# Kernel optimization log

Hardware: AMD Instinct MI355X
Metric: run time of the kernel (lower is better)

The kernel has to match this reference:

```python
import jax, jax.numpy as jnp
import numpy as np
from jax import lax

B, L, E, P, K, KS, H, T = 64, 512, 256, 64, 512, 3, 512, 53
V, MAXL = 50000, 512


def _span_idx(k):
    ks, kl = jax.random.split(k)
    starts = jax.random.randint(ks, (B,), 1, L - 9)
    spans = jax.random.randint(kl, (B,), 0, 8)
    return jnp.stack([starts, starts + spans], axis=1)  # [B,2], 1<=s<=e<L-1


def setup_inputs() -> dict:
    key = jax.random.key(0)
    ks = jax.random.split(key, 12)
    context = jax.random.randint(ks[0], (B, L), 0, V)
    subject_idx = _span_idx(ks[1])
    object_idx = _span_idx(ks[2])
    subject_dis = jax.random.randint(ks[3], (B, L), 0, 2 * MAXL)
    object_dis = jax.random.randint(ks[4], (B, L), 0, 2 * MAXL)
    embed_table = jax.random.normal(ks[5], (V, E), jnp.float32) * 0.02
    pos_table = jax.random.normal(ks[6], (2 * MAXL, P), jnp.float32) * 0.02
    Cin = 3 * E + 2 * P
    conv_w = jax.random.normal(ks[7], (K, Cin, KS), jnp.float32) * 0.02
    conv_b = jnp.zeros((K,), jnp.float32)
    lin1_w = jax.random.normal(ks[8], (H, K), jnp.float32) * 0.02
    lin1_b = jnp.zeros((H,), jnp.float32)
    lin2_w = jax.random.normal(ks[9], (T, 6 * E + H), jnp.float32) * 0.02
    lin2_b = jnp.zeros((T,), jnp.float32)
    return {"context": context, "subject_idx": subject_idx, "object_idx": object_idx,
            "subject_dis": subject_dis, "object_dis": object_dis,
            "embed_table": embed_table, "pos_table": pos_table,
            "conv_w": conv_w, "conv_b": conv_b,
            "lin1_w": lin1_w, "lin1_b": lin1_b, "lin2_w": lin2_w, "lin2_b": lin2_b}


def _entity_features(embed, idx):
    # embed: [B,L,E'], idx: [B,2] (start,end) inclusive span
    s, e = idx[:, 0], idx[:, 1]
    pos = jnp.arange(L)
    mask = (pos[None, :] >= s[:, None]) & (pos[None, :] <= e[:, None])  # [B,L]
    cnt = mask.sum(axis=1).astype(embed.dtype)[:, None]
    mean = jnp.einsum('ble,bl->be', embed, mask.astype(embed.dtype)) / cnt
    bidx = jnp.arange(embed.shape[0])
    left = embed[bidx, s - 1]                       # start>=1 always in data (torch: start>=0 branch)
    right_ok = (e + 1) < L
    right = jnp.where(right_ok[:, None], embed[bidx, jnp.clip(e + 1, 0, L - 1)], 0.0)
    return jnp.concatenate([mean, left, right], axis=1)  # [B,3E']


def reference(context, subject_idx, object_idx, subject_dis, object_dis,
              embed_table, pos_table, conv_w, conv_b,
              lin1_w, lin1_b, lin2_w, lin2_b):
    embed = embed_table[context]                    # [B,L,E]
    subj = _entity_features(embed, subject_idx)     # [B,3E]
    obj = _entity_features(embed, object_idx)       # [B,3E]

    # shift-and-concat window features (zero pad one step each side)
    epad = jnp.pad(embed, ((0, 0), (1, 1), (0, 0)))
    word = jnp.concatenate([epad[:, :-2], epad[:, 1:-1], epad[:, 2:]], axis=2)  # [B,L,3E]

    pos_feat = jnp.concatenate([pos_table[subject_dis], pos_table[object_dis]], axis=2)  # [B,L,2P]
    sent = jnp.concatenate([word, pos_feat], axis=2).transpose(0, 2, 1)  # [B,C,L]

    conv = lax.conv_general_dilated(sent, conv_w, window_strides=(1,),
                                    padding=[(KS // 2, KS // 2)],
                                    dimension_numbers=('NCH', 'OIH', 'NCH'))
    conv = conv + conv_b[None, :, None]             # [B,K,L]
    pooled = conv.max(axis=2)                       # global maxpool -> [B,K]
    sent_h = jnp.tanh(pooled @ lin1_w.T + lin1_b)   # [B,H]

    com = jnp.concatenate([subj, obj, sent_h], axis=1)  # [B,6E+H]
    scores = com @ lin2_w.T + lin2_b                # [B,T]; decode = argmax(scores, 1)
    return scores
```

## Files before the change

kernel.cpp:

```cpp
#include <hip/hip_runtime.h>
#include <hip/hip_bf16.h>
#include <hip/hip_fp8.h>
#include <stdint.h>

#define B_   64
#define L_   512
#define E_   256
#define P_   64
#define KOUT 512
#define KS_  3
#define H_   512
#define T_   53
#define CINW 2688
#define LE   516
#define LPP  514
#define COMW 2048

#define FP8_S    64.0f
#define DESCALE  (1.0f / 4096.0f)

#define SEC_CW    0
#define SEC_EMBP  512
#define SEC_POSP  (SEC_EMBP + (B_ * LE / 4))
#define SEC_ENT   (SEC_POSP + (B_ * LPP / 4))
#define SEC_POOL  (SEC_ENT + 2 * B_)
#define SEC_END   (SEC_POOL + 32)

typedef __attribute__((ext_vector_type(4))) float f32x4;
typedef __attribute__((ext_vector_type(4))) int   i32x4;
typedef __attribute__((ext_vector_type(8))) int   i32x8;

__device__ __forceinline__ unsigned enc_f(float x) {
    unsigned u = __float_as_uint(x);
    return (u & 0x80000000u) ? ~u : (u | 0x80000000u);
}
__device__ __forceinline__ float dec_f(unsigned e) {
    return __uint_as_float((e & 0x80000000u) ? (e & 0x7fffffffu) : ~e);
}
__device__ __forceinline__ unsigned char f8c(float x) {
    __hip_fp8_e4m3 t(x);
    return t.__x;
}

__device__ __forceinline__ void cp16(const void* g, void* l) {
    __builtin_amdgcn_global_load_lds(
        (const __attribute__((address_space(1))) unsigned int*)g,
        (__attribute__((address_space(3))) unsigned int*)l,
        16, 0, 0);
}

__global__ void prep(const float* __restrict__ conv_w,
                     const int* __restrict__ context,
                     const int* __restrict__ sidx,
                     const int* __restrict__ oidx,
                     const int* __restrict__ sdis,
                     const int* __restrict__ odis,
                     const float* __restrict__ etab,
                     const float* __restrict__ ptab,
                     unsigned char* __restrict__ wce,
                     unsigned char* __restrict__ wcp,
                     unsigned char* __restrict__ embp,
                     unsigned char* __restrict__ posp,
                     float* __restrict__ corr,
                     float* __restrict__ com,
                     unsigned* __restrict__ pooled) {
    __shared__ float w[CINW];
    const int blk = blockIdx.x;
    const int tid = threadIdx.x;

    if (blk < SEC_EMBP) {
        int n = blk;
        const float* src = conv_w + (size_t)n * CINW;
        for (int i = tid; i < CINW; i += 256) w[i] = src[i];
        __syncthreads();
        for (int i = tid; i < 5 * E_; i += 256) {
            int d = i >> 8, c = i & 255;
            float s = 0.f;
#pragma unroll
            for (int tau = 0; tau <= 2; tau++) {
                int seg = d - tau;
                if (seg >= 0 && seg <= 2) s += w[(seg * 256 + c) * 3 + tau];
            }
            wce[((size_t)d * KOUT + n) * E_ + c] = f8c(s * FP8_S);
        }
        for (int i = tid; i < 3 * 128; i += 256) {
            int tau = i >> 7, p = i & 127;
            wcp[((size_t)tau * KOUT + n) * 128 + p] = f8c(w[(768 + p) * 3 + tau] * FP8_S);
        }
        {
            int p   = tid >> 1, sub = tid & 1;
            int bb  = p >> 1, which = p & 1;
            int token = context[bb * L_ + (which ? L_ - 1 : 0)];
            const float4* er4 = (const float4*)(etab + (size_t)token * E_ + sub * 128);
            int A = which ? (sub * 384 + 2) : (1536 + sub * 384);
            float s = 0.f;
#pragma unroll 8
            for (int c4 = 0; c4 < 32; c4++) {
                float4 v = er4[c4];
                int c = c4 * 4;
                s += v.x * w[A + 3 * c]     + v.y * w[A + 3 * c + 3]
                   + v.z * w[A + 3 * c + 6] + v.w * w[A + 3 * c + 9];
            }
            s += __shfl_xor(s, 1, 64);
            if (sub == 0) corr[(bb * 2 + which) * KOUT + n] = s;
        }
    } else if (blk < SEC_POSP) {
        int row = (blk - SEC_EMBP) * 4 + (tid >> 6);
        int lane = tid & 63;
        int b = row / LE, r = row % LE;
        unsigned char* out = embp + (size_t)row * E_;
        if (r < 2 || r >= LE - 2) {
            *(uchar4*)(out + lane * 4) = (uchar4){0, 0, 0, 0};
            return;
        }
        int token = context[b * L_ + (r - 2)];
        float4 v = *(const float4*)(etab + (size_t)token * E_ + lane * 4);
        uchar4 pk;
        pk.x = f8c(v.x * FP8_S); pk.y = f8c(v.y * FP8_S);
        pk.z = f8c(v.z * FP8_S); pk.w = f8c(v.w * FP8_S);
        *(uchar4*)(out + lane * 4) = pk;
    } else if (blk < SEC_ENT) {
        int row = (blk - SEC_POSP) * 4 + (tid >> 6);
        int lane = tid & 63;
        int b = row / LPP, r = row % LPP;
        unsigned char* out = posp + (size_t)row * 128;
        if (r < 1 || r >= LPP - 1) {
            *(unsigned short*)(out + lane * 2) = 0;
            return;
        }
        int l = r - 1;
        int which = lane >> 5;
        int i2 = (lane & 31) * 2;
        int t = which ? odis[b * L_ + l] : sdis[b * L_ + l];
        float2 v = *(const float2*)(ptab + (size_t)t * P_ + i2);
        unsigned short pk = (unsigned short)f8c(v.x * FP8_S)
                          | ((unsigned short)f8c(v.y * FP8_S) << 8);
        *(unsigned short*)(out + which * 64 + i2) = pk;
    } else if (blk < SEC_POOL) {
        int idx = blk - SEC_ENT;
        int b = idx >> 1, which = idx & 1;
        const int* sp = which ? oidx : sidx;
        int s = sp[b * 2 + 0], e = sp[b * 2 + 1];
        const int* ctx = context + b * L_;
        float* outb = com + (size_t)b * COMW + which * 768;
        int d = tid;
        float sum = 0.f;
        for (int x = s; x <= e; ++x) sum += etab[(size_t)ctx[x] * E_ + d];
        outb[d] = sum / (float)(e - s + 1);
        outb[256 + d] = etab[(size_t)ctx[s - 1] * E_ + d];
        float r = 0.f;
        if (e + 1 < L_) r = etab[(size_t)ctx[e + 1] * E_ + d];
        outb[512 + d] = r;
    } else {
        int base = ((blk - SEC_POOL) * 256 + tid) * 4;
        *(uint4*)(pooled + base) = (uint4){0, 0, 0, 0};
    }
}

__global__ void __launch_bounds__(256, 3)
conv_gemm_pool(const unsigned char* __restrict__ embp,
               const unsigned char* __restrict__ posp,
               const unsigned char* __restrict__ wce,
               const unsigned char* __restrict__ wcp,
               const float* __restrict__ corr,
               unsigned* __restrict__ pooled) {
    __shared__ unsigned char winA[136 * 128];
    __shared__ unsigned char sB[2][128 * 128];

    const int tid  = threadIdx.x;
    const int lane = tid & 63;
    const int wave = tid >> 6;
    const int mt = blockIdx.x;
    const int nt = blockIdx.y;
    const int b  = mt >> 2;
    const int l0 = (mt & 3) * 128;
    const int n0 = nt * 128;

    const int wr = (wave & 1) * 64;
    const int wc = (wave >> 1) * 64;
    const int m  = lane & 15;
    const int q  = lane >> 4;

    f32x4 acc[4][4];
#pragma unroll
    for (int i = 0; i < 4; i++)
#pragma unroll
        for (int j = 0; j < 4; j++) acc[i][j] = (f32x4){0.f, 0.f, 0.f, 0.f};

    const int srow = tid >> 3;
    const int ssw  = ((tid & 7) ^ (srow & 7)) << 4;
    auto stageB = [&](int buf, int t) {
        const unsigned char* base; int stride;
        if (t < 10) {
            int tap = (t < 5) ? t : t - 5;
            int kc  = (t < 5) ? 0 : 128;
            base = wce + (size_t)(tap * KOUT + n0) * E_ + kc;
            stride = E_;
        } else {
            int tap = t - 10;
            base = wcp + (size_t)(tap * KOUT + n0) * 128;
            stride = 128;
        }
        char* dB = (char*)sB[buf] + tid * 16;
#pragma unroll
        for (int rnd = 0; rnd < 4; rnd++)
            cp16(base + (srow + rnd * 32) * stride + ssw, dB + rnd * 4096);
    };

    auto stageWin = [&](const unsigned char* base, int stride) {
#pragma unroll
        for (int k = 0; k < 4; k++) {
            int idx = tid + k * 256;
            int r = idx >> 3, c = idx & 7;
            cp16(base + r * stride + ((c ^ (r & 7)) << 4), (char*)winA + idx * 16);
        }
        if (tid < 64) {
            int idx = tid + 1024;
            int r = idx >> 3, c = idx & 7;
            cp16(base + r * stride + ((c ^ (r & 7)) << 4), (char*)winA + idx * 16);
        }
    };

    auto frag = [&](const unsigned char* rowbase, int row) -> i32x8 {
        const unsigned char* rp = rowbase + row * 128;
        int x = (row & 7) << 4;
        i32x4 lo = *(const i32x4*)(rp + (((q << 1) << 4) ^ x));
        i32x4 hi = *(const i32x4*)(rp + ((((q << 1) | 1) << 4) ^ x));
        return (i32x8){lo[0], lo[1], lo[2], lo[3], hi[0], hi[1], hi[2], hi[3]};
    };

    auto compute = [&](int buf, int tap) {
        i32x8 af[4];
#pragma unroll
        for (int i = 0; i < 4; i++) af[i] = frag(winA, tap + wr + i * 16 + m);
#pragma unroll
        for (int j = 0; j < 4; j++) {
            i32x8 bfv = frag(sB[buf], wc + j * 16 + m);
#pragma unroll
            for (int i = 0; i < 4; i++)
                acc[i][j] = __builtin_amdgcn_mfma_scale_f32_16x16x128_f8f6f4(
                    af[i], bfv, acc[i][j], 0, 0, 0, 0x7f7f7f7f, 0, 0x7f7f7f7f);
        }
    };

    stageWin(embp + (size_t)(b * LE + l0) * E_, E_);
    stageB(0, 0);
    asm volatile("s_waitcnt vmcnt(0)" ::: "memory");
    __builtin_amdgcn_s_barrier();

    int cur = 0;
#pragma unroll 1
    for (int t = 0; t < 13; t++) {
        bool pend = (t == 4 || t == 9);
        if (t < 12 && !pend) {
            stageB(cur ^ 1, t + 1);
            asm volatile("s_waitcnt vmcnt(4)" ::: "memory");
        } else {
            asm volatile("s_waitcnt vmcnt(0)" ::: "memory");
        }
        __builtin_amdgcn_s_barrier();
        __builtin_amdgcn_sched_barrier(0);
        compute(cur, (t < 5) ? t : (t < 10 ? t - 5 : t - 10));
        __builtin_amdgcn_sched_barrier(0);
        __builtin_amdgcn_s_barrier();
        if (pend) {
            if (t == 4) stageWin(embp + (size_t)(b * LE + l0) * E_ + 128, E_);
            else        stageWin(posp + (size_t)(b * LPP + l0) * 128, 128);
            stageB(cur ^ 1, t + 1);
            asm volatile("s_waitcnt vmcnt(0)" ::: "memory");
            __builtin_amdgcn_s_barrier();
        }
        cur ^= 1;
    }

    const float* corrb = corr + b * 2 * KOUT;
#pragma unroll
    for (int j = 0; j < 4; j++) {
        int col = n0 + wc + j * 16 + m;
        float mx = -3.4e38f;
#pragma unroll
        for (int i = 0; i < 4; i++)
#pragma unroll
            for (int r = 0; r < 4; r++) {
                float v = acc[i][j][r] * DESCALE;
                int l = l0 + wr + i * 16 + q * 4 + r;
                if (l == 0)      v -= corrb[col];
                if (l == L_ - 1) v -= corrb[KOUT + col];
                mx = fmaxf(mx, v);
            }
        mx = fmaxf(mx, __shfl_xor(mx, 16, 64));
        mx = fmaxf(mx, __shfl_xor(mx, 32, 64));
        if (q == 0) atomicMax(&pooled[b * KOUT + col], enc_f(mx));
    }
}

__global__ void lin1_k(const unsigned* __restrict__ pooled,
                       const float* __restrict__ conv_b,
                       const float* __restrict__ lin1_w,
                       const float* __restrict__ lin1_b,
                       float* __restrict__ com) {
    int bid = blockIdx.x;
    int wave = threadIdx.x >> 6, lane = threadIdx.x & 63;
    int b = bid >> 7;
    int h = (bid & 127) * 4 + wave;
    const float* w = lin1_w + (size_t)h * KOUT;
    const unsigned* pb = pooled + b * KOUT;
    float s = 0.f;
#pragma unroll
    for (int i = 0; i < 8; i++) {
        int k = lane + 64 * i;
        s += (dec_f(pb[k]) + conv_b[k]) * w[k];
    }
#pragma unroll
    for (int off = 32; off > 0; off >>= 1) s += __shfl_down(s, off, 64);
    if (lane == 0) com[(size_t)b * COMW + 1536 + h] = tanhf(s + lin1_b[h]);
}

__global__ void lin2_k(const float* __restrict__ com,
                       const float* __restrict__ lin2_w,
                       const float* __restrict__ lin2_b,
                       float* __restrict__ out) {
    int b = blockIdx.x;
    int wave = threadIdx.x >> 6, lane = threadIdx.x & 63;
    int t = blockIdx.y * 4 + wave;
    if (t >= T_) return;
    const float* w = lin2_w + (size_t)t * COMW;
    const float* c = com + (size_t)b * COMW;
    float s = 0.f;
#pragma unroll
    for (int i = 0; i < 32; i++) {
        int k = lane + 64 * i;
        s += c[k] * w[k];
    }
#pragma unroll
    for (int off = 32; off > 0; off >>= 1) s += __shfl_down(s, off, 64);
    if (lane == 0) out[b * T_ + t] = s + lin2_b[t];
}

extern "C" void kernel_launch(void* const* d_in, const int* in_sizes, int n_in,
                              void* d_out, int out_size, void* d_ws, size_t ws_size,
                              hipStream_t stream) {
    const int*   context = (const int*)d_in[0];
    const int*   sidx    = (const int*)d_in[1];
    const int*   oidx    = (const int*)d_in[2];
    const int*   sdis    = (const int*)d_in[3];
    const int*   odis    = (const int*)d_in[4];
    const float* etab    = (const float*)d_in[5];
    const float* ptab    = (const float*)d_in[6];
    const float* conv_w  = (const float*)d_in[7];
    const float* conv_b  = (const float*)d_in[8];
    const float* lin1_w  = (const float*)d_in[9];
    const float* lin1_b  = (const float*)d_in[10];
    const float* lin2_w  = (const float*)d_in[11];
    const float* lin2_b  = (const float*)d_in[12];
    float* out = (float*)d_out;

    char* ws = (char*)d_ws;
    size_t off = 0;
    unsigned char* embp = (unsigned char*)(ws + off);
    off += (size_t)B_ * LE * E_;
    off = (off + 255) & ~(size_t)255;
    unsigned char* posp = (unsigned char*)(ws + off);
    off += (size_t)B_ * LPP * 128;
    off = (off + 255) & ~(size_t)255;
    unsigned char* wce = (unsigned char*)(ws + off);
    off += (size_t)5 * KOUT * E_;
    off = (off + 255) & ~(size_t)255;
    unsigned char* wcp = (unsigned char*)(ws + off);
    off += (size_t)3 * KOUT * 128;
    off = (off + 255) & ~(size_t)255;
    float* corr = (float*)(ws + off);
    off += (size_t)B_ * 2 * KOUT * 4;
    off = (off + 255) & ~(size_t)255;
    unsigned* pooled = (unsigned*)(ws + off);
    off += (size_t)B_ * KOUT * 4;
    off = (off + 255) & ~(size_t)255;
    float* com = (float*)(ws + off);
    off += (size_t)B_ * COMW * 4;

    prep<<<dim3(SEC_END), dim3(256), 0, stream>>>(
        conv_w, context, sidx, oidx, sdis, odis, etab, ptab,
        wce, wcp, embp, posp, corr, com, pooled);
    conv_gemm_pool<<<dim3(256, 4), dim3(256), 0, stream>>>(embp, posp, wce, wcp, corr, pooled);
    lin1_k<<<dim3(8192), dim3(256), 0, stream>>>(pooled, conv_b, lin1_w, lin1_b, com);
    lin2_k<<<dim3(B_, 14), dim3(256), 0, stream>>>(com, lin2_w, lin2_b, out);
}
```

Baseline: 184.9 us.

## Load conv weight fragments directly into registers and double-buffer activation tiles in LDS

The conv GEMM kernel used to keep a shared activation window (136 rows) that was reused across taps, with weight tiles staged through LDS. It now loads the weight B-fragments straight from global memory into registers, double-buffered across iterations, and stages a fresh 128x128 activation tile per tap/k-chunk into double-buffered LDS. This removes the window reload stalls at t=4 and t=9 and cuts LDS usage to 32KB, which may raise occupancy. In exchange it re-fetches overlapping activation rows for every tap, does uncoalesced per-lane global weight loads (32B per lane), and holds more registers for the two B-fragment sets.

```diff
diff --git a/kernel.cpp b/kernel.cpp
--- a/kernel.cpp
+++ b/kernel.cpp
@@ -164,8 +164,7 @@
                const unsigned char* __restrict__ wcp,
                const float* __restrict__ corr,
                unsigned* __restrict__ pooled) {
-    __shared__ unsigned char winA[136 * 128];
-    __shared__ unsigned char sB[2][128 * 128];
+    __shared__ unsigned char sA[2][128 * 128];
 
     const int tid  = threadIdx.x;
     const int lane = tid & 63;
@@ -189,11 +188,27 @@
 
     const int srow = tid >> 3;
     const int ssw  = ((tid & 7) ^ (srow & 7)) << 4;
-    auto stageB = [&](int buf, int t) {
+    auto stageA = [&](int buf, int t) {
         const unsigned char* base; int stride;
         if (t < 10) {
-            int tap = (t < 5) ? t : t - 5;
-            int kc  = (t < 5) ? 0 : 128;
+            int tap = t >> 1, kc = (t & 1) << 7;
+            base = embp + (size_t)(b * LE + l0 + tap) * E_ + kc;
+            stride = E_;
+        } else {
+            int tap = t - 10;
+            base = posp + (size_t)(b * LPP + l0 + tap) * 128;
+            stride = 128;
+        }
+        char* d = (char*)sA[buf] + tid * 16;
+#pragma unroll
+        for (int rnd = 0; rnd < 4; rnd++)
+            cp16(base + (srow + rnd * 32) * stride + ssw, d + rnd * 4096);
+    };
+
+    auto loadB = [&](int t, i32x8* bn) {
+        const unsigned char* base; int stride;
+        if (t < 10) {
+            int tap = t >> 1, kc = (t & 1) << 7;
             base = wce + (size_t)(tap * KOUT + n0) * E_ + kc;
             stride = E_;
         } else {
@@ -201,27 +216,16 @@
             base = wcp + (size_t)(tap * KOUT + n0) * 128;
             stride = 128;
         }
-        char* dB = (char*)sB[buf] + tid * 16;
-#pragma unroll
-        for (int rnd = 0; rnd < 4; rnd++)
-            cp16(base + (srow + rnd * 32) * stride + ssw, dB + rnd * 4096);
+#pragma unroll
+        for (int j = 0; j < 4; j++) {
+            const unsigned char* rp = base + (size_t)(wc + j * 16 + m) * stride + q * 32;
+            i32x4 lo = *(const i32x4*)rp;
+            i32x4 hi = *(const i32x4*)(rp + 16);
+            bn[j] = (i32x8){lo[0], lo[1], lo[2], lo[3], hi[0], hi[1], hi[2], hi[3]};
+        }
     };
 
-    auto stageWin = [&](const unsigned char* base, int stride) {
-#pragma unroll
-        for (int k = 0; k < 4; k++) {
-            int idx = tid + k * 256;
-            int r = idx >> 3, c = idx & 7;
-            cp16(base + r * stride + ((c ^ (r & 7)) << 4), (char*)winA + idx * 16);
-        }
-        if (tid < 64) {
-            int idx = tid + 1024;
-            int r = idx >> 3, c = idx & 7;
-            cp16(base + r * stride + ((c ^ (r & 7)) << 4), (char*)winA + idx * 16);
-        }
-    };
-
-    auto frag = [&](const unsigned char* rowbase, int row) -> i32x8 {
+    auto fragA = [&](const unsigned char* rowbase, int row) -> i32x8 {
         const unsigned char* rp = rowbase + row * 128;
         int x = (row & 7) << 4;
         i32x4 lo = *(const i32x4*)(rp + (((q << 1) << 4) ^ x));
@@ -229,48 +233,39 @@
         return (i32x8){lo[0], lo[1], lo[2], lo[3], hi[0], hi[1], hi[2], hi[3]};
     };
 
-    auto compute = [&](int buf, int tap) {
-        i32x8 af[4];
-#pragma unroll
-        for (int i = 0; i < 4; i++) af[i] = frag(winA, tap + wr + i * 16 + m);
-#pragma unroll
-        for (int j = 0; j < 4; j++) {
-            i32x8 bfv = frag(sB[buf], wc + j * 16 + m);
-#pragma unroll
-            for (int i = 0; i < 4; i++)
+    auto compute = [&](int buf, i32x8* bc) {
+#pragma unroll
+        for (int i = 0; i < 4; i++) {
+            i32x8 af = fragA(sA[buf], wr + i * 16 + m);
+#pragma unroll
+            for (int j = 0; j < 4; j++)
                 acc[i][j] = __builtin_amdgcn_mfma_scale_f32_16x16x128_f8f6f4(
-                    af[i], bfv, acc[i][j], 0, 0, 0, 0x7f7f7f7f, 0, 0x7f7f7f7f);
+                    af, bc[j], acc[i][j], 0, 0, 0, 0x7f7f7f7f, 0, 0x7f7f7f7f);
         }
     };
 
-    stageWin(embp + (size_t)(b * LE + l0) * E_, E_);
-    stageB(0, 0);
+    i32x8 b0[4], b1[4];
+    loadB(0, b0);
+    stageA(0, 0);
     asm volatile("s_waitcnt vmcnt(0)" ::: "memory");
     __builtin_amdgcn_s_barrier();
 
-    int cur = 0;
-#pragma unroll 1
+#pragma unroll
     for (int t = 0; t < 13; t++) {
-        bool pend = (t == 4 || t == 9);
-        if (t < 12 && !pend) {
-            stageB(cur ^ 1, t + 1);
-            asm volatile("s_waitcnt vmcnt(4)" ::: "memory");
+        i32x8* bc = (t & 1) ? b1 : b0;
+        i32x8* bn = (t & 1) ? b0 : b1;
+        if (t < 12) {
+            loadB(t + 1, bn);
+            stageA((t + 1) & 1, t + 1);
+            asm volatile("s_waitcnt vmcnt(12)" ::: "memory");
         } else {
             asm volatile("s_waitcnt vmcnt(0)" ::: "memory");
         }
         __builtin_amdgcn_s_barrier();
         __builtin_amdgcn_sched_barrier(0);
-        compute(cur, (t < 5) ? t : (t < 10 ? t - 5 : t - 10));
+        compute(t & 1, bc);
         __builtin_amdgcn_sched_barrier(0);
         __builtin_amdgcn_s_barrier();
-        if (pend) {
-            if (t == 4) stageWin(embp + (size_t)(b * LE + l0) * E_ + 128, E_);
-            else        stageWin(posp + (size_t)(b * LPP + l0) * 128, 128);
-            stageB(cur ^ 1, t + 1);
-            asm volatile("s_waitcnt vmcnt(0)" ::: "memory");
-            __builtin_amdgcn_s_barrier();
-        }
-        cur ^= 1;
     }
 
     const float* corrb = corr + b * 2 * KOUT;
```

Measured after the change: 470.5 us. 154% more time.
